# Performance work log

Measured on AMD Instinct MI355X. Metric: run time of the kernel, lower is better.

The kernel has to match this reference:

```python
import math
import jax, jax.numpy as jnp
import numpy as np

HID, HEADS, HEAD_DIM, MLP = 768, 12, 64, 3072
ROT_AXIS = HEAD_DIM // 4  # 16 rotary dims per spatial axis, 48 total
MAX_FREQ = 256.0
EPS_GN, EPS_LN = 1e-6, 1e-5


def setup_inputs() -> dict:
    key = jax.random.key(0)
    ks = jax.random.split(key, 5)
    B, H, W, D = 2, 12, 12, 12
    s = 0.02
    return {
        "x": jax.random.normal(ks[0], (B, HID, H, W, D), jnp.float32),
        "norm1_w": jnp.ones((HID,), jnp.float32),
        "w_fused": jax.random.normal(ks[1], (MLP + 3 * HID, HID), jnp.float32) * s,
        "b_fused": jnp.zeros((MLP + 3 * HID,), jnp.float32),
        "q_gamma": jnp.ones((HEAD_DIM,), jnp.float32),
        "q_beta": jnp.zeros((HEAD_DIM,), jnp.float32),
        "k_gamma": jnp.ones((HEAD_DIM,), jnp.float32),
        "k_beta": jnp.zeros((HEAD_DIM,), jnp.float32),
        "w_attn": jax.random.normal(ks[2], (HID, HID), jnp.float32) * s,
        "w_ff": jax.random.normal(ks[3], (HID, MLP // 2), jnp.float32) * s,
        "b_ff": jnp.zeros((HID,), jnp.float32),
    }


def _layernorm(t, gamma, beta):
    mu = jnp.mean(t, axis=-1, keepdims=True)
    var = jnp.mean((t - mu) ** 2, axis=-1, keepdims=True)
    return (t - mu) / jnp.sqrt(var + EPS_LN) * gamma + beta


def _rotate_half(t):
    # interleaved pairs: (x1, x2) -> (-x2, x1)
    t2 = t.reshape(t.shape[:-1] + (t.shape[-1] // 2, 2))
    return jnp.stack((-t2[..., 1], t2[..., 0]), axis=-1).reshape(t.shape)


def _axial_freqs(H, W, D):
    base = jnp.linspace(1.0, MAX_FREQ / 2, ROT_AXIS // 2) * math.pi  # (8,)
    def ax(n):
        pos = jnp.linspace(-1.0, 1.0, n)
        f = pos[:, None] * base[None, :]          # (n, 8)
        return jnp.repeat(f, 2, axis=-1)          # (n, 16)
    fH = jnp.broadcast_to(ax(H)[:, None, None, :], (H, W, D, ROT_AXIS))
    fW = jnp.broadcast_to(ax(W)[None, :, None, :], (H, W, D, ROT_AXIS))
    fD = jnp.broadcast_to(ax(D)[None, None, :, :], (H, W, D, ROT_AXIS))
    return jnp.concatenate((fH, fW, fD), axis=-1)  # (H, W, D, 48)


def _apply_rope(t, cosf, sinf, rot_dim):
    t_mid, t_right = t[..., :rot_dim], t[..., rot_dim:]
    t_mid = t_mid * cosf + _rotate_half(t_mid) * sinf
    return jnp.concatenate((t_mid, t_right), axis=-1)


def reference(x, norm1_w, w_fused, b_fused, q_gamma, q_beta, k_gamma, k_beta,
              w_attn, w_ff, b_ff):
    B, C, H, W, D = x.shape
    residual = x
    # RMSGroupNorm: norm axes are the spatial dims only (per-channel RMS)
    rms = jnp.sqrt(jnp.mean(x ** 2, axis=(2, 3, 4), keepdims=True) + EPS_GN)
    xn = x / rms * norm1_w[None, :, None, None, None]
    xn = jnp.transpose(xn, (0, 2, 3, 4, 1))  # b h w d c
    fused = jnp.einsum('bhwdc,oc->bhwdo', xn, w_fused) + b_fused
    ff = fused[..., :MLP]
    q = fused[..., MLP:MLP + HID]
    k = fused[..., MLP + HID:MLP + 2 * HID]
    v = fused[..., MLP + 2 * HID:]
    def to_heads(t):  # b h w d (he c) -> b he h w d c
        return jnp.transpose(t.reshape(B, H, W, D, HEADS, HEAD_DIM), (0, 4, 1, 2, 3, 5))
    q, k, v = to_heads(q), to_heads(k), to_heads(v)
    q = _layernorm(q, q_gamma, q_beta)
    k = _layernorm(k, k_gamma, k_beta)
    freqs = _axial_freqs(H, W, D)                 # (H, W, D, 48)
    cosf, sinf = jnp.cos(freqs), jnp.sin(freqs)
    rot_dim = freqs.shape[-1]
    q = _apply_rope(q, cosf, sinf, rot_dim)
    k = _apply_rope(k, cosf, sinf, rot_dim)
    S = H * W * D
    q = q.reshape(B, HEADS, S, HEAD_DIM)
    k = k.reshape(B, HEADS, S, HEAD_DIM)
    v = v.reshape(B, HEADS, S, HEAD_DIM)
    scale = 1.0 / math.sqrt(HEAD_DIM)
    attn = jax.nn.softmax(jnp.einsum('bhsc,bhtc->bhst', q, k) * scale, axis=-1)
    att = jnp.einsum('bhst,bhtc->bhsc', attn, v)
    att = jnp.transpose(att, (0, 2, 1, 3)).reshape(B, H, W, D, HID)
    attn_out = jnp.einsum('bhwdc,oc->bhwdo', att, w_attn)
    ff_x, gate = jnp.split(ff, 2, axis=-1)
    ff_act = jax.nn.silu(gate) * ff_x
    ff_out = jnp.einsum('bhwdc,oc->bhwdo', ff_act, w_ff) + b_ff
    out = attn_out + ff_out
    out = jnp.transpose(out, (0, 4, 1, 2, 3)) + residual
    return out
```

## Files before the change

kernel.cpp:

```cpp
#include <hip/hip_runtime.h>

using bf16 = __bf16;
typedef __attribute__((ext_vector_type(8))) __bf16 bf16x8;
typedef __attribute__((ext_vector_type(4))) float f32x4;

#define HID    768
#define S_TOT  1728
#define MLP_   3072
#define NFUSED 5376
#define HEADS  12
#define HDIM   64
#define ROT    48
#define KCAT   2304
#define NQKV   2304

__device__ __forceinline__ void gload16(const void* g, void* l) {
  __builtin_amdgcn_global_load_lds((__attribute__((address_space(1))) void*)g,
                                   (__attribute__((address_space(3))) void*)l,
                                   16, 0, 0);
}

__device__ __forceinline__ float fexp2(float x) {
  float r; asm("v_exp_f32 %0, %1" : "=v"(r) : "v"(x)); return r;
}

__device__ __forceinline__ unsigned int cvtpk(float lo, float hi) {
  unsigned int r;
  asm("v_cvt_pk_bf16_f32 %0, %1, %2" : "=v"(r) : "v"(lo), "v"(hi));
  return r;
}

__device__ __forceinline__ float wsum64(float v) {
  #pragma unroll
  for (int d = 32; d; d >>= 1) v += __shfl_xor(v, d);
  return v;
}

__global__ __launch_bounds__(256) void k_conv(const float* __restrict__ wf,
    const float* __restrict__ wa, const float* __restrict__ wff,
    const float* __restrict__ bfu,
    bf16* __restrict__ owf, bf16* __restrict__ wcat, float* __restrict__ bperm) {
  int i = blockIdx.x * 256 + threadIdx.x;
  const int nf = NFUSED * HID, na = HID * HID, nff = HID * (MLP_ / 2);
  auto perm = [](int o) {
    if (o < 1536) return (o >> 4) * 32 + (o & 15);
    if (o < 3072) { int g = o - 1536; return (g >> 4) * 32 + 16 + (g & 15); }
    return o;
  };
  if (i < nf) {
    int o = i / HID, c = i % HID;
    owf[(size_t)perm(o) * HID + c] = (bf16)wf[i];
  }
  if (i < NFUSED) bperm[perm(i)] = bfu[i];
  if (i < na)  wcat[(i / HID) * KCAT + (i % HID)] = (bf16)wa[i];
  if (i < nff) wcat[(i / (MLP_ / 2)) * KCAT + HID + (i % (MLP_ / 2))] = (bf16)wff[i];
}

__global__ __launch_bounds__(256) void k_rms(const float* __restrict__ x,
    const float* __restrict__ w, float* __restrict__ scale) {
  int bc = blockIdx.x;
  const float* xp = x + (size_t)bc * S_TOT;
  float s = 0.f;
  for (int i = threadIdx.x; i < S_TOT; i += 256) { float v = xp[i]; s += v * v; }
  s = wsum64(s);
  __shared__ float red[4];
  int lane = threadIdx.x & 63, wv = threadIdx.x >> 6;
  if (lane == 0) red[wv] = s;
  __syncthreads();
  if (threadIdx.x == 0) {
    float t = red[0] + red[1] + red[2] + red[3];
    scale[bc] = w[bc % HID] * rsqrtf(t * (1.f / S_TOT) + 1e-6f);
  }
}

__global__ __launch_bounds__(256) void k_xpose(const float* __restrict__ x,
    const float* __restrict__ scale, bf16* __restrict__ xn) {
  __shared__ float t[32][33];
  int b = blockIdx.z, st = blockIdx.x * 32, ct = blockIdx.y * 32;
  int tx = threadIdx.x & 31, ty = threadIdx.x >> 5;
  #pragma unroll
  for (int i = 0; i < 4; ++i) {
    int c = ct + ty + i * 8;
    t[ty + i * 8][tx] = x[((size_t)b * HID + c) * S_TOT + st + tx] * scale[b * HID + c];
  }
  __syncthreads();
  #pragma unroll
  for (int i = 0; i < 4; ++i) {
    int s = st + ty + i * 8;
    xn[((size_t)b * S_TOT + s) * HID + ct + tx] = (bf16)t[tx][ty + i * 8];
  }
}

__global__ __launch_bounds__(256) void k_rope(float* __restrict__ ct, float* __restrict__ st) {
  int i = blockIdx.x * 256 + threadIdx.x;
  if (i >= S_TOT * ROT) return;
  int s = i / ROT, j = i % ROT;
  int axis = j >> 4, pr = (j & 15) >> 1;
  float base = 3.14159265358979323846f * (1.f + pr * (127.f / 7.f));
  int coord = axis == 0 ? (s / 144) : axis == 1 ? ((s / 12) % 12) : (s % 12);
  float pos = -1.f + coord * (2.f / 11.f);
  float f = pos * base;
  ct[i] = cosf(f); st[i] = sinf(f);
}

__global__ __launch_bounds__(256, 3) void k_gemmF(const bf16* __restrict__ A,
    const bf16* __restrict__ Bw, const float* __restrict__ bias,
    bf16* __restrict__ acat, bf16* __restrict__ qkvb, int M, int N, int K) {
  extern __shared__ __align__(16) char smem[];
  bf16* aL = (bf16*)smem;
  bf16* bL = (bf16*)(smem + 2 * 8192);
  constexpr int BN = 192, NT = 6;
  const int nT = K / 32;
  int nwg = gridDim.x;
  int cq = nwg >> 3, crr = nwg & 7;
  int xcd = blockIdx.x & 7, pos = blockIdx.x >> 3;
  int idx = (xcd < crr ? xcd * (cq + 1) : crr * (cq + 1) + (xcd - crr) * cq) + pos;
  int nmt = M / 128;
  int n0 = (idx / nmt) * BN, m0 = (idx % nmt) * 128;
  int lane = threadIdx.x & 63, wv = threadIdx.x >> 6;
  int wm = (wv >> 1) * 64, wn = (wv & 1) * (BN / 2);
  int arow = lane >> 2;
  int acs = ((lane & 3) ^ ((lane >> 3) & 3)) * 8;
  int r16 = lane & 15, g8 = (lane >> 4) * 8;
  int swz = ((r16 >> 1) & 3) << 3;
  const bf16* Ag = A + (size_t)m0 * K;
  const bf16* Bg = Bw + (size_t)n0 * K;
  auto stage = [&](int p, int t) {
    int kk = t * 32;
    #pragma unroll
    for (int i = 0; i < 2; ++i) {
      int rb = wv * 32 + i * 16;
      gload16(Ag + (size_t)(rb + arow) * K + kk + acs, aL + p * 4096 + rb * 32);
    }
    #pragma unroll
    for (int i = 0; i < 3; ++i) {
      int rb = wv * 48 + i * 16;
      gload16(Bg + (size_t)(rb + arow) * K + kk + acs, bL + p * (BN * 32) + rb * 32);
    }
  };
  f32x4 acc[4][NT] = {};
  int p = 0;
  stage(0, 0);
  for (int t = 0; t < nT; ++t) {
    if (t + 1 < nT) {
      stage(p ^ 1, t + 1);
      asm volatile("s_waitcnt vmcnt(5)\ns_barrier" ::: "memory");
    } else {
      asm volatile("s_waitcnt vmcnt(0)\ns_barrier" ::: "memory");
    }
    bf16x8 af[4];
    #pragma unroll
    for (int mi = 0; mi < 4; ++mi)
      af[mi] = *(const bf16x8*)(aL + p * 4096 + (wm + mi * 16 + r16) * 32 + (g8 ^ swz));
    __builtin_amdgcn_s_setprio(1);
    #pragma unroll
    for (int ni = 0; ni < NT; ++ni) {
      bf16x8 bfr = *(const bf16x8*)(bL + p * (BN * 32) + (wn + ni * 16 + r16) * 32 + (g8 ^ swz));
      #pragma unroll
      for (int mi = 0; mi < 4; ++mi)
        acc[mi][ni] = __builtin_amdgcn_mfma_f32_16x16x32_bf16(af[mi], bfr, acc[mi][ni], 0, 0, 0);
    }
    __builtin_amdgcn_s_setprio(0);
    asm volatile("s_barrier" ::: "memory");
    p ^= 1;
  }
  int cr = (lane >> 4) * 4;
  if (n0 < MLP_) {
    #pragma unroll
    for (int pp = 0; pp < 3; ++pp) {
      int base = n0 + wn + pp * 32;
      int ch = (base >> 5) * 16 + r16;
      float bx = bias[base + r16], bg = bias[base + 16 + r16];
      #pragma unroll
      for (int mi = 0; mi < 4; ++mi)
        #pragma unroll
        for (int j = 0; j < 4; ++j) {
          int row = m0 + wm + mi * 16 + cr + j;
          float xv = acc[mi][2 * pp][j] + bx;
          float gv = acc[mi][2 * pp + 1][j] + bg;
          float sg = gv / (1.f + fexp2(gv * -1.442695041f));
          acat[(size_t)row * KCAT + HID + ch] = (bf16)(sg * xv);
        }
    }
  } else {
    #pragma unroll
    for (int mi = 0; mi < 4; ++mi)
      #pragma unroll
      for (int ni = 0; ni < NT; ++ni) {
        int col = n0 + wn + ni * 16 + r16;
        float bv = bias[col];
        #pragma unroll
        for (int j = 0; j < 4; ++j) {
          int row = m0 + wm + mi * 16 + cr + j;
          qkvb[(size_t)row * NQKV + (col - MLP_)] = (bf16)(acc[mi][ni][j] + bv);
        }
      }
  }
}

__global__ __launch_bounds__(256, 3) void k_gemmO(const bf16* __restrict__ A,
    const bf16* __restrict__ Bw, const float* __restrict__ bias,
    float* __restrict__ Out, const float* __restrict__ X, int M, int N, int K) {
  extern __shared__ __align__(16) char smem[];
  bf16* aL = (bf16*)smem;
  bf16* bL = (bf16*)(smem + 2 * 16384);
  const int nT = K / 64;
  int nwg = gridDim.x;
  int cq = nwg >> 3, crr = nwg & 7;
  int xcd = blockIdx.x & 7, pos = blockIdx.x >> 3;
  int idx = (xcd < crr ? xcd * (cq + 1) : crr * (cq + 1) + (xcd - crr) * cq) + pos;
  int ntn = N / 64;
  int m0 = (idx / ntn) * 128, n0 = (idx % ntn) * 64;
  int lane = threadIdx.x & 63, wv = threadIdx.x >> 6;
  int wm = (wv >> 1) * 64, wn = (wv & 1) * 32;
  int rg = lane >> 3, ch = lane & 7;
  int scs = (ch ^ rg) * 8;
  int r16 = lane & 15, g8 = (lane >> 4) * 8;
  const bf16* Ag = A + (size_t)m0 * K;
  const bf16* Bg = Bw + (size_t)n0 * K;
  auto stage = [&](int p, int t) {
    int kk = t * 64;
    #pragma unroll
    for (int i = 0; i < 4; ++i) {
      int rb = wv * 32 + i * 8;
      gload16(Ag + (size_t)(rb + rg) * K + kk + scs, aL + p * 8192 + rb * 64);
    }
    #pragma unroll
    for (int i = 0; i < 2; ++i) {
      int rb = wv * 16 + i * 8;
      gload16(Bg + (size_t)(rb + rg) * K + kk + scs, bL + p * 4096 + rb * 64);
    }
  };
  f32x4 acc[4][2] = {};
  int p = 0;
  stage(0, 0);
  for (int t = 0; t < nT; ++t) {
    if (t + 1 < nT) {
      stage(p ^ 1, t + 1);
      asm volatile("s_waitcnt vmcnt(6)\ns_barrier" ::: "memory");
    } else {
      asm volatile("s_waitcnt vmcnt(0)\ns_barrier" ::: "memory");
    }
    bf16x8 af[4][2], bfr[2][2];
    #pragma unroll
    for (int kc = 0; kc < 2; ++kc) {
      int ce = ((kc * 4 + (lane >> 4)) ^ (r16 & 7)) * 8;
      #pragma unroll
      for (int mi = 0; mi < 4; ++mi)
        af[mi][kc] = *(const bf16x8*)(aL + p * 8192 + (wm + mi * 16 + r16) * 64 + ce);
      #pragma unroll
      for (int ni = 0; ni < 2; ++ni)
        bfr[ni][kc] = *(const bf16x8*)(bL + p * 4096 + (wn + ni * 16 + r16) * 64 + ce);
    }
    __builtin_amdgcn_s_setprio(1);
    #pragma unroll
    for (int kc = 0; kc < 2; ++kc)
      #pragma unroll
      for (int mi = 0; mi < 4; ++mi)
        #pragma unroll
        for (int ni = 0; ni < 2; ++ni)
          acc[mi][ni] = __builtin_amdgcn_mfma_f32_16x16x32_bf16(af[mi][kc], bfr[ni][kc], acc[mi][ni], 0, 0, 0);
    __builtin_amdgcn_s_setprio(0);
    asm volatile("s_barrier" ::: "memory");
    p ^= 1;
  }
  int cr = (lane >> 4) * 4;
  float* tb = (float*)smem;
  __syncthreads();
  #pragma unroll
  for (int mi = 0; mi < 4; ++mi)
    #pragma unroll
    for (int ni = 0; ni < 2; ++ni) {
      int c = wn + ni * 16 + r16;
      float bv = bias[n0 + c];
      #pragma unroll
      for (int j = 0; j < 4; ++j)
        tb[c * 129 + wm + mi * 16 + cr + j] = acc[mi][ni][j] + bv;
    }
  __syncthreads();
  for (int ci = 0; ci < 16; ++ci) {
    int c = wv * 16 + ci;
    #pragma unroll
    for (int si = 0; si < 2; ++si) {
      int r = si * 64 + lane;
      int m = m0 + r;
      int bb = (m >= S_TOT) ? 1 : 0;
      size_t oidx = ((size_t)bb * HID + n0 + c) * S_TOT + (m - bb * S_TOT);
      Out[oidx] = tb[c * 129 + r] + X[oidx];
    }
  }
}

__global__ __launch_bounds__(256) void k_qkv(const bf16* __restrict__ qkvb,
    const float* __restrict__ ct, const float* __restrict__ st,
    const float* __restrict__ qg, const float* __restrict__ qb,
    const float* __restrict__ kg, const float* __restrict__ kb,
    bf16* __restrict__ qr, bf16* __restrict__ kr, bf16* __restrict__ vt) {
  int bs = blockIdx.x;
  int b = bs / S_TOT, s = bs % S_TOT;
  int lane = threadIdx.x & 63, wv = threadIdx.x >> 6;
  int d = lane;
  float c = 0.f, sn = 0.f;
  if (d < ROT) { c = ct[s * ROT + d]; sn = st[s * ROT + d]; }
  for (int it = 0; it < 9; ++it) {
    int rr = wv * 9 + it;
    int t = rr / HEADS, h = rr % HEADS;
    float v = (float)qkvb[(size_t)bs * NQKV + t * HID + h * HDIM + d];
    if (t < 2) {
      float s1 = v, s2 = v * v;
      #pragma unroll
      for (int dd = 32; dd; dd >>= 1) { s1 += __shfl_xor(s1, dd); s2 += __shfl_xor(s2, dd); }
      float mu = s1 * (1.f / 64);
      float var = s2 * (1.f / 64) - mu * mu;
      float vn = (v - mu) * rsqrtf(var + 1e-5f);
      vn = (t == 0) ? (vn * qg[d] + qb[d]) : (vn * kg[d] + kb[d]);
      float o = vn;
      if (d < ROT) {
        float p = __shfl_xor(vn, 1);
        float rot = (d & 1) ? p : -p;
        o = vn * c + rot * sn;
      }
      if (t == 0) o *= 0.18033688f;
      bf16* dst = (t == 0) ? qr : kr;
      dst[((size_t)(b * HEADS + h) * S_TOT + s) * HDIM + d] = (bf16)o;
    } else {
      int sl = s & 63;
      int sp = (s & ~63) | ((sl & 15) << 2) | (sl >> 4);
      vt[((size_t)(b * HEADS + h) * HDIM + d) * S_TOT + sp] = (bf16)v;
    }
  }
}

__global__ __launch_bounds__(256, 4) void k_attn(const bf16* __restrict__ qr,
    const bf16* __restrict__ kr, const bf16* __restrict__ vt, bf16* __restrict__ acat) {
  __shared__ __align__(16) bf16 kld[2][4096];
  __shared__ __align__(16) bf16 vld[2][4096];
  __shared__ __align__(16) bf16 pld[4][1024];
  int rid = (blockIdx.x & 7) * 81 + (blockIdx.x >> 3);
  int bh = rid / 27, qt = rid % 27;
  int lane = threadIdx.x & 63, wv = threadIdx.x >> 6;
  int r16 = lane & 15, g8 = (lane >> 4) * 8;
  int sw = (r16 & 7) << 3;
  int lsw = (lane & 56) | ((lane ^ (lane >> 3)) & 7);
  const bf16* qbase = qr + ((size_t)bh * S_TOT + qt * 64 + wv * 16) * HDIM;
  bf16x8 qf[2];
  qf[0] = *(const bf16x8*)(qbase + r16 * HDIM + g8);
  qf[1] = *(const bf16x8*)(qbase + r16 * HDIM + 32 + g8);
  asm volatile("s_waitcnt vmcnt(0)" ::: "memory");
  const bf16* kg0 = kr + (size_t)bh * S_TOT * HDIM;
  const bf16* vg0 = vt + (size_t)bh * HDIM * S_TOT;
  auto stage = [&](int buf, int kt) {
    #pragma unroll
    for (int i = 0; i < 2; ++i) {
      int q = wv * 2 + i;
      gload16(kg0 + (size_t)kt * 4096 + q * 512 + lsw * 8, &kld[buf][q * 512]);
      gload16(vg0 + (size_t)(q * 8 + (lane >> 3)) * S_TOT + kt * 64 + (lsw & 7) * 8,
              &vld[buf][q * 512]);
    }
  };
  float l_part[4] = {0.f, 0.f, 0.f, 0.f};
  f32x4 acc_o[4] = {};
  stage(0, 0);
  int buf = 0;
  for (int kt = 0; kt < 27; ++kt) {
    asm volatile("s_waitcnt vmcnt(0)\ns_barrier" ::: "memory");
    if (kt + 1 < 27) stage(buf ^ 1, kt + 1);
    f32x4 sa[4];
    __builtin_amdgcn_s_setprio(1);
    #pragma unroll
    for (int nt = 0; nt < 4; ++nt) {
      sa[nt] = f32x4{0.f, 0.f, 0.f, 0.f};
      #pragma unroll
      for (int kc = 0; kc < 2; ++kc) {
        bf16x8 kf = *(const bf16x8*)(&kld[buf][(nt * 16 + r16) * 64 + ((kc * 32 + g8) ^ sw)]);
        sa[nt] = __builtin_amdgcn_mfma_f32_16x16x32_bf16(qf[kc], kf, sa[nt], 0, 0, 0);
      }
    }
    __builtin_amdgcn_s_setprio(0);
    #pragma unroll
    for (int j = 0; j < 4; ++j) {
      #pragma unroll
      for (int nt = 0; nt < 4; ++nt) {
        float pv = fexp2(sa[nt][j]);
        sa[nt][j] = pv;
        l_part[j] += pv;
      }
    }
    #pragma unroll
    for (int j = 0; j < 4; ++j) {
      int rr = (lane >> 4) * 4 + j;
      unsigned int pa = cvtpk(sa[0][j], sa[1][j]);
      unsigned int pb = cvtpk(sa[2][j], sa[3][j]);
      unsigned long long pk = (unsigned long long)pa | ((unsigned long long)pb << 32);
      int off = rr * 64 + ((4 * r16) ^ ((rr & 7) << 3));
      *(unsigned long long*)(&pld[wv][off]) = pk;
    }
    __builtin_amdgcn_s_setprio(1);
    #pragma unroll
    for (int nt = 0; nt < 4; ++nt)
      #pragma unroll
      for (int kc = 0; kc < 2; ++kc) {
        bf16x8 pf = *(const bf16x8*)(&pld[wv][r16 * 64 + ((kc * 32 + g8) ^ sw)]);
        bf16x8 vf = *(const bf16x8*)(&vld[buf][(nt * 16 + r16) * 64 + ((kc * 32 + g8) ^ sw)]);
        acc_o[nt] = __builtin_amdgcn_mfma_f32_16x16x32_bf16(pf, vf, acc_o[nt], 0, 0, 0);
      }
    __builtin_amdgcn_s_setprio(0);
    buf ^= 1;
  }
  int b = bh / HEADS, h = bh % HEADS;
  #pragma unroll
  for (int j = 0; j < 4; ++j) {
    float l = l_part[j];
    #pragma unroll
    for (int dd = 1; dd < 16; dd <<= 1) l += __shfl_xor(l, dd);
    float inv = 1.f / l;
    int s = qt * 64 + wv * 16 + (lane >> 4) * 4 + j;
    #pragma unroll
    for (int nt = 0; nt < 4; ++nt)
      acat[((size_t)b * S_TOT + s) * KCAT + h * HDIM + nt * 16 + r16] = (bf16)(acc_o[nt][j] * inv);
  }
}

extern "C" void kernel_launch(void* const* d_in, const int* in_sizes, int n_in,
                              void* d_out, int out_size, void* d_ws, size_t ws_size,
                              hipStream_t stream) {
  const float* x   = (const float*)d_in[0];
  const float* n1w = (const float*)d_in[1];
  const float* wf  = (const float*)d_in[2];
  const float* bfu = (const float*)d_in[3];
  const float* qg  = (const float*)d_in[4];
  const float* qb  = (const float*)d_in[5];
  const float* kg  = (const float*)d_in[6];
  const float* kb  = (const float*)d_in[7];
  const float* wa  = (const float*)d_in[8];
  const float* wff = (const float*)d_in[9];
  const float* bff = (const float*)d_in[10];
  float* out = (float*)d_out;

  char* ws = (char*)d_ws;
  size_t off = 0;
  auto alloc = [&](size_t bytes) {
    void* p = ws + off;
    off = (off + bytes + 255) & ~(size_t)255;
    return p;
  };
  const int M = 2 * S_TOT;
  bf16*  wf_b   = (bf16*)alloc((size_t)NFUSED * HID * 2);
  bf16*  wcat   = (bf16*)alloc((size_t)HID * KCAT * 2);
  float* bperm  = (float*)alloc((size_t)NFUSED * 4);
  float* scale  = (float*)alloc(2 * HID * 4);
  bf16*  xn     = (bf16*)alloc((size_t)M * HID * 2);
  float* ctab   = (float*)alloc((size_t)S_TOT * ROT * 4);
  float* stab   = (float*)alloc((size_t)S_TOT * ROT * 4);
  bf16*  qkvb   = (bf16*)alloc((size_t)M * NQKV * 2);
  bf16*  qrb    = (bf16*)alloc((size_t)24 * S_TOT * HDIM * 2);
  bf16*  krb    = (bf16*)alloc((size_t)24 * S_TOT * HDIM * 2);
  bf16*  vtb    = (bf16*)alloc((size_t)24 * HDIM * S_TOT * 2);
  bf16*  acat   = (bf16*)alloc((size_t)M * KCAT * 2);
  if (off > ws_size) return;

  const int LDS_QKV = 2 * 8192 + 2 * 192 * 32 * 2;
  const int LDS_MRG = 2 * 16384 + 2 * 8192;
  hipFuncSetAttribute((const void*)k_gemmF, hipFuncAttributeMaxDynamicSharedMemorySize, LDS_QKV);
  hipFuncSetAttribute((const void*)k_gemmO, hipFuncAttributeMaxDynamicSharedMemorySize, LDS_MRG);

  k_conv<<<(NFUSED * HID + 255) / 256, 256, 0, stream>>>(wf, wa, wff, bfu, wf_b, wcat, bperm);
  k_rms<<<2 * HID, 256, 0, stream>>>(x, n1w, scale);
  k_xpose<<<dim3(S_TOT / 32, HID / 32, 2), 256, 0, stream>>>(x, scale, xn);
  k_rope<<<(S_TOT * ROT + 255) / 256, 256, 0, stream>>>(ctab, stab);
  k_gemmF<<<(M / 128) * (NFUSED / 192), 256, LDS_QKV, stream>>>(
      xn, wf_b, bperm, acat, qkvb, M, NFUSED, HID);
  k_qkv<<<M, 256, 0, stream>>>(qkvb, ctab, stab, qg, qb, kg, kb, qrb, krb, vtb);
  k_attn<<<648, 256, 0, stream>>>(qrb, krb, vtb, acat);
  k_gemmO<<<(M / 128) * (HID / 64), 256, LDS_MRG, stream>>>(
      acat, wcat, bff, out, x, M, HID, KCAT);
}
```

Baseline: 139.9 us.

## Software-pipeline attention loop: compute next tile's QK^T before current softmax/PV

Splits the K and V staging so K tiles are prefetched two iterations ahead and V tiles one ahead. The QK^T MFMAs for tile kt+1 are issued before the exp, bf16 pack and PV work for tile kt. The aim is to overlap the matrix-core work with the transcendental and LDS work, and to hide load latency. In exchange it keeps a second set of score registers live, which raises VGPR pressure under the 4-waves launch bound and could cause spills.

```diff
diff --git a/kernel.cpp b/kernel.cpp
--- a/kernel.cpp
+++ b/kernel.cpp
@@ -349,48 +349,61 @@
   asm volatile("s_waitcnt vmcnt(0)" ::: "memory");
   const bf16* kg0 = kr + (size_t)bh * S_TOT * HDIM;
   const bf16* vg0 = vt + (size_t)bh * HDIM * S_TOT;
-  auto stage = [&](int buf, int kt) {
+  auto stageK = [&](int bp, int kt) {
     #pragma unroll
     for (int i = 0; i < 2; ++i) {
       int q = wv * 2 + i;
-      gload16(kg0 + (size_t)kt * 4096 + q * 512 + lsw * 8, &kld[buf][q * 512]);
+      gload16(kg0 + (size_t)kt * 4096 + q * 512 + lsw * 8, &kld[bp][q * 512]);
+    }
+  };
+  auto stageV = [&](int bp, int kt) {
+    #pragma unroll
+    for (int i = 0; i < 2; ++i) {
+      int q = wv * 2 + i;
       gload16(vg0 + (size_t)(q * 8 + (lane >> 3)) * S_TOT + kt * 64 + (lsw & 7) * 8,
-              &vld[buf][q * 512]);
-    }
+              &vld[bp][q * 512]);
+    }
+  };
+  auto qkt = [&](int bp, f32x4* sa) {
+    __builtin_amdgcn_s_setprio(1);
+    #pragma unroll
+    for (int nt = 0; nt < 4; ++nt) {
+      sa[nt] = f32x4{0.f, 0.f, 0.f, 0.f};
+      #pragma unroll
+      for (int kc = 0; kc < 2; ++kc) {
+        bf16x8 kf = *(const bf16x8*)(&kld[bp][(nt * 16 + r16) * 64 + ((kc * 32 + g8) ^ sw)]);
+        sa[nt] = __builtin_amdgcn_mfma_f32_16x16x32_bf16(qf[kc], kf, sa[nt], 0, 0, 0);
+      }
+    }
+    __builtin_amdgcn_s_setprio(0);
   };
   float l_part[4] = {0.f, 0.f, 0.f, 0.f};
   f32x4 acc_o[4] = {};
-  stage(0, 0);
+  f32x4 s_cur[4], s_nx[4];
+  stageK(0, 0); stageV(0, 0);
+  stageK(1, 1);
+  asm volatile("s_waitcnt vmcnt(2)\ns_barrier" ::: "memory");
+  qkt(0, s_cur);
   int buf = 0;
   for (int kt = 0; kt < 27; ++kt) {
     asm volatile("s_waitcnt vmcnt(0)\ns_barrier" ::: "memory");
-    if (kt + 1 < 27) stage(buf ^ 1, kt + 1);
-    f32x4 sa[4];
-    __builtin_amdgcn_s_setprio(1);
-    #pragma unroll
-    for (int nt = 0; nt < 4; ++nt) {
-      sa[nt] = f32x4{0.f, 0.f, 0.f, 0.f};
-      #pragma unroll
-      for (int kc = 0; kc < 2; ++kc) {
-        bf16x8 kf = *(const bf16x8*)(&kld[buf][(nt * 16 + r16) * 64 + ((kc * 32 + g8) ^ sw)]);
-        sa[nt] = __builtin_amdgcn_mfma_f32_16x16x32_bf16(qf[kc], kf, sa[nt], 0, 0, 0);
-      }
-    }
-    __builtin_amdgcn_s_setprio(0);
+    if (kt < 26) stageV(buf ^ 1, kt + 1);
+    if (kt < 25) stageK(buf, kt + 2);
+    if (kt < 26) qkt(buf ^ 1, s_nx);
     #pragma unroll
     for (int j = 0; j < 4; ++j) {
       #pragma unroll
       for (int nt = 0; nt < 4; ++nt) {
-        float pv = fexp2(sa[nt][j]);
-        sa[nt][j] = pv;
+        float pv = fexp2(s_cur[nt][j]);
+        s_cur[nt][j] = pv;
         l_part[j] += pv;
       }
     }
     #pragma unroll
     for (int j = 0; j < 4; ++j) {
       int rr = (lane >> 4) * 4 + j;
-      unsigned int pa = cvtpk(sa[0][j], sa[1][j]);
-      unsigned int pb = cvtpk(sa[2][j], sa[3][j]);
+      unsigned int pa = cvtpk(s_cur[0][j], s_cur[1][j]);
+      unsigned int pb = cvtpk(s_cur[2][j], s_cur[3][j]);
       unsigned long long pk = (unsigned long long)pa | ((unsigned long long)pb << 32);
       int off = rr * 64 + ((4 * r16) ^ ((rr & 7) << 3));
       *(unsigned long long*)(&pld[wv][off]) = pk;
@@ -405,6 +418,10 @@
         acc_o[nt] = __builtin_amdgcn_mfma_f32_16x16x32_bf16(pf, vf, acc_o[nt], 0, 0, 0);
       }
     __builtin_amdgcn_s_setprio(0);
+    if (kt < 26) {
+      #pragma unroll
+      for (int nt = 0; nt < 4; ++nt) s_cur[nt] = s_nx[nt];
+    }
     buf ^= 1;
   }
   int b = bh / HEADS, h = bh % HEADS;
```

Result: no change. 141.3 us (+1.0%).
